# Kernel tuning notes

Measured on AMD Instinct MI355X. Metric: run time of the kernel, lower is better.

The kernel has to match this reference:

```python
import jax, jax.numpy as jnp
import numpy as np

B, N = 4, 8192
D = 128
DEPTH = 4
LEAF = 32
HEADS = 4
HD = D // HEADS
SLOTS = 24
RANKS = [20, 32, 52, 82]                      # rank at encoder step j (fine -> coarse)
EXP = [RANKS[j] * (2 ** j) for j in range(DEPTH)]  # HODLR head output dims


def _rope_tables(seq_len, dim):
    inv_freq = 1.0 / (10000.0 ** (jnp.arange(0, dim, 2, dtype=jnp.float32) / dim))
    t = jnp.arange(seq_len, dtype=jnp.float32)
    freqs = t[:, None] * inv_freq[None, :]
    emb = jnp.concatenate([freqs, freqs], axis=-1)   # [S, dim]
    return jnp.cos(emb), jnp.sin(emb)


def _rotate_half(x):
    x1, x2 = jnp.split(x, 2, axis=-1)
    return jnp.concatenate([-x2, x1], axis=-1)


def _layernorm(x, g, b, eps=1e-5):
    mu = jnp.mean(x, -1, keepdims=True)
    var = jnp.mean((x - mu) ** 2, -1, keepdims=True)
    return (x - mu) * jax.lax.rsqrt(var + eps) * g + b


def _block_attn(h, qkv_w, qkv_b, pw, pb, cos, sin):
    Bc, Nc, C = h.shape
    nb = Nc // LEAF
    xb = h.reshape(Bc * nb, LEAF, C)
    qkv = (xb @ qkv_w + qkv_b).reshape(Bc * nb, LEAF, 3, HEADS, HD)
    qkv = qkv.transpose(2, 0, 3, 1, 4)               # [3, BN, H, L, hd]
    q, k, v = qkv[0], qkv[1], qkv[2]
    q = q * cos + _rotate_half(q) * sin              # full-dim RoPE (rope_dim == head_dim)
    k = k * cos + _rotate_half(k) * sin
    attn = jax.nn.softmax(jnp.einsum('bhqd,bhkd->bhqk', q, k) * (HD ** -0.5), axis=-1)
    o = jnp.einsum('bhqk,bhkd->bhqd', attn, v).transpose(0, 2, 1, 3).reshape(Bc * nb, LEAF, C)
    return (o @ pw + pb).reshape(Bc, Nc, C)


def _forward(x, cen_w, cen_b, nbr_w, nbr_b, inp_w, inp_b,
             leafp_w, leafp_b, leafh_w, leafh_b, log_scale_leaf,
             ln1_g, ln1_b, qkv_w, qkv_b, attnp_w, attnp_b,
             ln2_g, ln2_b, mlp1_w, mlp1_b, mlp2_w, mlp2_b, ds_w, ds_b,
             hu_w0, hu_b0, hv_w0, hv_b0, hu_w1, hu_b1, hv_w1, hv_b1,
             hu_w2, hu_b2, hv_w2, hv_b2, hu_w3, hu_b3, hv_w3, hv_b3):
    Bx, Nx, _ = x.shape
    # --- SymmetricNeighborEmbed (24 neighbor slots, vectorized) ---
    pos_i = x[..., 0:3]
    diag_i = x[..., 3:4]
    h_center = jnp.concatenate([pos_i, diag_i], -1) @ cen_w + cen_b          # [B,N,D]
    nb_feat = x[..., 4:4 + 5 * SLOTS].reshape(Bx, Nx, SLOTS, 5)
    rel = nb_feat[..., 0:1]
    pos_j = nb_feat[..., 1:4]
    w_ij = nb_feat[..., 4:5]
    active = (w_ij != 0.0).astype(x.dtype)
    feat = jnp.concatenate([rel * active, (pos_j - pos_i[:, :, None, :]) * active, w_ij], -1)
    e = (feat @ nbr_w + nbr_b) * active                                       # [B,N,24,D]
    h = h_center + jnp.sum(e, axis=2)
    h = h @ inp_w + inp_b
    # --- leaf dense diagonal blocks ---
    nl = Nx // LEAF
    hl = h.reshape(Bx, nl, LEAF, D) @ leafp_w + leafp_b                       # [B,nl,32,32]
    u_leaf = hl @ leafh_w + leafh_b
    dense = jnp.einsum('blik,bljk->blij', u_leaf, u_leaf) * jnp.exp(log_scale_leaf)
    diag_a = x[..., 3]                                                        # scale_A defaults to 1.0
    mask = jnp.abs(diag_a) > 1e-6
    new_diag = jnp.where(mask, 1.0 / jnp.where(mask, diag_a, 1.0), 1.0).reshape(Bx, nl, LEAF)
    dense = dense + new_diag[..., :, None] * jnp.eye(LEAF, dtype=x.dtype)
    # --- down-only encoder: transformer block -> HODLR head -> 2:1 downsample ---
    cos, sin = _rope_tables(LEAF, HD)
    hu = [(hu_w0, hu_b0), (hu_w1, hu_b1), (hu_w2, hu_b2), (hu_w3, hu_b3)]
    hv = [(hv_w0, hv_b0), (hv_w1, hv_b1), (hv_w2, hv_b2), (hv_w3, hv_b3)]
    us, vs = [], []
    for j in range(DEPTH):
        a = _block_attn(_layernorm(h, ln1_g[j], ln1_b[j]),
                        qkv_w[j], qkv_b[j], attnp_w[j], attnp_b[j], cos, sin)
        h = h + a
        m = _layernorm(h, ln2_g[j], ln2_b[j])
        m = jax.nn.gelu(m @ mlp1_w[j] + mlp1_b[j], approximate=False) @ mlp2_w[j] + mlp2_b[j]
        h = h + m
        us.append((h @ hu[j][0] + hu[j][1]).reshape(Bx, Nx, RANKS[j]))
        vs.append((h @ hv[j][0] + hv[j][1]).reshape(Bx, Nx, RANKS[j]))
        Bh, n, c = h.shape
        h = h.reshape(Bh, n // 2, 2 * c) @ ds_w[j] + ds_b[j]
    # single flat output: dense leaf blocks + all U/V HODLR factors
    return jnp.concatenate([dense.reshape(Bx, -1),
                            jnp.concatenate(us, -1).reshape(Bx, -1),
                            jnp.concatenate(vs, -1).reshape(Bx, -1)], -1)


def setup_inputs():
    key = jax.random.key(0)
    ks = iter(jax.random.split(key, 64))
    def rn(shape, s=0.05):
        return jax.random.normal(next(ks), shape, jnp.float32) * s
    z = lambda *s: jnp.zeros(s, jnp.float32)
    o = lambda *s: jnp.ones(s, jnp.float32)
    inp = {
        'x': jax.random.normal(next(ks), (B, N, 4 + 5 * SLOTS), jnp.float32),
        'cen_w': rn((4, D)), 'cen_b': z(D),
        'nbr_w': rn((5, D)), 'nbr_b': z(D),
        'inp_w': rn((D, D)), 'inp_b': z(D),
        'leafp_w': rn((D, LEAF)), 'leafp_b': z(LEAF),
        'leafh_w': rn((LEAF, LEAF), 0.01), 'leafh_b': z(LEAF),
        'log_scale_leaf': jnp.full((1,), np.log(0.01), jnp.float32),
        'ln1_g': o(DEPTH, D), 'ln1_b': z(DEPTH, D),
        'qkv_w': rn((DEPTH, D, 3 * D)), 'qkv_b': z(DEPTH, 3 * D),
        'attnp_w': rn((DEPTH, D, D)), 'attnp_b': z(DEPTH, D),
        'ln2_g': o(DEPTH, D), 'ln2_b': z(DEPTH, D),
        'mlp1_w': rn((DEPTH, D, 4 * D)), 'mlp1_b': z(DEPTH, 4 * D),
        'mlp2_w': rn((DEPTH, 4 * D, D)), 'mlp2_b': z(DEPTH, D),
        'ds_w': rn((DEPTH, 2 * D, D)), 'ds_b': z(DEPTH, D),
    }
    for j in range(DEPTH):
        inp['hu_w%d' % j] = rn((D, EXP[j]), 0.01)
        inp['hu_b%d' % j] = z(EXP[j])
        inp['hv_w%d' % j] = rn((D, EXP[j]), 0.01)
        inp['hv_b%d' % j] = z(EXP[j])
    return inp


def reference(x, cen_w, cen_b, nbr_w, nbr_b, inp_w, inp_b,
              leafp_w, leafp_b, leafh_w, leafh_b, log_scale_leaf,
              ln1_g, ln1_b, qkv_w, qkv_b, attnp_w, attnp_b,
              ln2_g, ln2_b, mlp1_w, mlp1_b, mlp2_w, mlp2_b, ds_w, ds_b,
              hu_w0, hu_b0, hv_w0, hv_b0, hu_w1, hu_b1, hv_w1, hv_b1,
              hu_w2, hu_b2, hv_w2, hv_b2, hu_w3, hu_b3, hv_w3, hv_b3):
    return _forward(x, cen_w, cen_b, nbr_w, nbr_b, inp_w, inp_b,
                    leafp_w, leafp_b, leafh_w, leafh_b, log_scale_leaf,
                    ln1_g, ln1_b, qkv_w, qkv_b, attnp_w, attnp_b,
                    ln2_g, ln2_b, mlp1_w, mlp1_b, mlp2_w, mlp2_b, ds_w, ds_b,
                    hu_w0, hu_b0, hv_w0, hv_b0, hu_w1, hu_b1, hv_w1, hv_b1,
                    hu_w2, hu_b2, hv_w2, hv_b2, hu_w3, hu_b3, hv_w3, hv_b3)
```

## Files before the change

### kernel.cpp

```cpp
#include <hip/hip_runtime.h>
#include <hip/hip_bf16.h>
#include <math.h>

#define DEV __device__ __forceinline__

constexpr int XFv = 124;
constexpr size_t OPB   = 3309568;
constexpr size_t UBASE = 262144;
constexpr size_t VBASE = 1785856;
constexpr int UVWID = 186;

using bfrag  = __attribute__((ext_vector_type(8))) short;
using f32x4v = __attribute__((ext_vector_type(4))) float;

DEV float* at4p(float* base, int t, int c0, int W) {
  return base + t * W + ((c0 + 4 * t) & (W - 1));
}
DEV float& at1r(float* base, int t, int c, int W) {
  return base[t * W + (((c & ~3) + 4 * t) & (W - 1)) + (c & 3)];
}
DEV float4 ld4g(const float* p) { return *(const float4*)p; }
DEV void fma4(float4& a, float s, const float4& w) {
  a.x += s * w.x; a.y += s * w.y; a.z += s * w.z; a.w += s * w.w;
}
DEV float gelu_fast(float x) {
  float x2 = x * x;
  float z = x * (1.5957691216057308f + 0.0713551f * x2);
  float e = __expf(z);
  float r = 1.0f - __frcp_rn(e + 1.0f);
  return x * r;
}
DEV ushort f2bf(float x) {
  __hip_bfloat16 b = __float2bfloat16(x);
  union { __hip_bfloat16 h; ushort u; } cv;
  cv.h = b;
  return cv.u;
}
DEV unsigned f2bf2(float lo, float hi) {
  __hip_bfloat162 b2 = __float22bfloat162_rn(make_float2(lo, hi));
  union { __hip_bfloat162 h; unsigned u; } cv;
  cv.h = b2;
  return cv.u;
}
DEV void stb128(ushort* b, int row, int col, float v) {
  b[row * 128 + (((col & ~7) + 8 * row) & 127) + (col & 7)] = f2bf(v);
}

__global__ __launch_bounds__(256) void wprep_all_kernel(
    const float* __restrict__ src0, ushort* __restrict__ dst0, int K, int N) {
  size_t off = (size_t)blockIdx.z * K * N;
  const float* src = src0 + off;
  ushort* dst = dst0 + off;
  __shared__ float S[64][65];
  int tid = threadIdx.x;
  int k0 = blockIdx.x * 64, n0 = blockIdx.y * 64;
  for (int i = tid; i < 64 * 64; i += 256) {
    int kk = i >> 6, nn = i & 63;
    S[kk][nn] = src[(size_t)(k0 + kk) * N + n0 + nn];
  }
  __syncthreads();
  int n = tid >> 2, kq = tid & 3;
  unsigned pk[8];
#pragma unroll
  for (int i = 0; i < 8; i++) {
    int k = kq * 16 + 2 * i;
    pk[i] = f2bf2(S[k][n], S[k + 1][n]);
  }
  unsigned* dp = (unsigned*)&dst[(size_t)(n0 + n) * K + k0 + kq * 16];
#pragma unroll
  for (int i = 0; i < 8; i++) dp[i] = pk[i];
}

struct UVDesc {
  const float* src[8];
  ushort* dst[8];
  int expj[8];
  int npad[8];
};
__global__ __launch_bounds__(256) void uvprep_all_kernel(UVDesc d) {
  int mi = blockIdx.y;
  int i = blockIdx.x * 256 + threadIdx.x;
  int expj = d.expj[mi];
  if (i >= d.npad[mi] * 128) return;
  int n = i >> 7, k = i & 127;
  d.dst[mi][(size_t)n * 128 + k] =
      (n < expj) ? f2bf(d.src[mi][(size_t)k * expj + n]) : (ushort)0;
}

__global__ __launch_bounds__(128) void weff_prep_kernel(
    const float* __restrict__ cw, const float* __restrict__ cb,
    const float* __restrict__ nw, const float* __restrict__ nb,
    const float* __restrict__ iw, const float* __restrict__ ib,
    float* __restrict__ weff, float* __restrict__ ropetab) {
  __shared__ float S[11 * 128];
  int tid = threadIdx.x;
  for (int i = tid; i < 512; i += 128) S[i] = cw[i];
  for (int i = tid; i < 640; i += 128) S[512 + i] = nw[i];
  S[1152 + tid] = nb[tid];
  S[1280 + tid] = cb[tid];
  __syncthreads();
  float acc[11];
#pragma unroll
  for (int r = 0; r < 10; r++) acc[r] = 0.f;
  acc[10] = ib[tid];
  for (int k = 0; k < 128; k++) {
    float w = iw[k * 128 + tid];
#pragma unroll
    for (int r = 0; r < 11; r++) acc[r] += S[r * 128 + k] * w;
  }
#pragma unroll
  for (int r = 0; r < 11; r++) weff[r * 128 + tid] = acc[r];
  for (int idx = tid; idx < 512; idx += 128) {
    int pos = idx >> 4, d = idx & 15;
    float ang = (float)pos * expf(-0.57564627324851148f * (float)d);
    ropetab[idx] = cosf(ang);
    ropetab[512 + idx] = sinf(ang);
  }
}

__global__ __launch_bounds__(256) void node_embed2_kernel(
    const float* __restrict__ x, const float* __restrict__ weff,
    float* __restrict__ h) {
  __shared__ float XR[64 * XFv];
  __shared__ float RF[64][11];
  __shared__ __align__(16) float WE[11 * 128];
  int tid = threadIdx.x;
  int node0 = blockIdx.x * 64;
  for (int i = tid; i < 64 * XFv; i += 256)
    XR[i] = x[(size_t)node0 * XFv + i];
  for (int i = tid; i < 11 * 128; i += 256) WE[i] = weff[i];
  __syncthreads();
  {
    int nn = tid >> 2, sl = tid & 3;
    const float* xr = XR + nn * XFv;
    float p0 = xr[0], p1 = xr[1], p2 = xr[2];
    float g[6] = {0.f, 0.f, 0.f, 0.f, 0.f, 0.f};
#pragma unroll
    for (int s = 0; s < 6; s++) {
      const float* f = xr + 4 + 5 * (sl * 6 + s);
      float w = f[4];
      if (w != 0.0f) {
        g[0] += f[0]; g[1] += f[1] - p0; g[2] += f[2] - p1;
        g[3] += f[3] - p2; g[4] += w; g[5] += 1.0f;
      }
    }
#pragma unroll
    for (int i = 0; i < 6; i++) {
      g[i] += __shfl_xor(g[i], 1);
      g[i] += __shfl_xor(g[i], 2);
    }
    if (sl == 0) {
      RF[nn][0] = p0; RF[nn][1] = p1; RF[nn][2] = p2; RF[nn][3] = xr[3];
#pragma unroll
      for (int i = 0; i < 6; i++) RF[nn][4 + i] = g[i];
    }
  }
  __syncthreads();
  {
    int w = tid >> 6, lane = tid & 63;
    int c4 = lane & 31, hi = lane >> 5;
    const float4* WE4 = (const float4*)WE;
#pragma unroll
    for (int rr = 0; rr < 8; rr++) {
      int node = w * 16 + rr * 2 + hi;
      float4 acc = WE4[10 * 32 + c4];
#pragma unroll
      for (int f = 0; f < 10; f++)
        fma4(acc, RF[node][f], WE4[f * 32 + c4]);
      *(float4*)&h[(size_t)(node0 + node) * 128 + c4 * 4] = acc;
    }
  }
}

__global__ __launch_bounds__(256) void leaf_dense_kernel(
    const float* __restrict__ h, const float* __restrict__ x,
    const float* __restrict__ lpw, const float* __restrict__ lpb,
    const float* __restrict__ lhw, const float* __restrict__ lhb,
    const float* __restrict__ lsc, float* __restrict__ out) {
  __shared__ __align__(16) float HS[32 * 128];
  __shared__ __align__(16) float HL[32 * 32];
  __shared__ __align__(16) float UL[32 * 32];
  int tid = threadIdx.x;
  int leaf = blockIdx.x;
  size_t base = (size_t)leaf * (32 * 128);
  for (int i = tid; i < 32 * 128; i += 256) {
    int t = i >> 7, c = i & 127;
    at1r(HS, t, c, 128) = h[base + i];
  }
  __syncthreads();
  int t = tid & 31, cg = tid >> 5;
  {
    float4 acc = ld4g(&lpb[4 * cg]);
    for (int k4 = 0; k4 < 128; k4 += 4) {
      float4 xv = *(const float4*)at4p(HS, t, k4, 128);
      float xa[4] = {xv.x, xv.y, xv.z, xv.w};
#pragma unroll
      for (int kk = 0; kk < 4; kk++)
        fma4(acc, xa[kk], ld4g(&lpw[(k4 + kk) * 32 + 4 * cg]));
    }
    *(float4*)at4p(HL, t, 4 * cg, 32) = acc;
  }
  __syncthreads();
  {
    float4 acc = ld4g(&lhb[4 * cg]);
    for (int k4 = 0; k4 < 32; k4 += 4) {
      float4 xv = *(const float4*)at4p(HL, t, k4, 32);
      float xa[4] = {xv.x, xv.y, xv.z, xv.w};
#pragma unroll
      for (int kk = 0; kk < 4; kk++)
        fma4(acc, xa[kk], ld4g(&lhw[(k4 + kk) * 32 + 4 * cg]));
    }
    *(float4*)at4p(UL, t, 4 * cg, 32) = acc;
  }
  __syncthreads();
  {
    float scale = expf(lsc[0]);
    float acc[4] = {0.f, 0.f, 0.f, 0.f};
    for (int k4 = 0; k4 < 32; k4 += 4) {
      float4 xv = *(const float4*)at4p(UL, t, k4, 32);
      float xa[4] = {xv.x, xv.y, xv.z, xv.w};
#pragma unroll
      for (int kk = 0; kk < 4; kk++) {
        int k = k4 + kk;
#pragma unroll
        for (int i2 = 0; i2 < 4; i2++)
          acc[i2] += xa[kk] * at1r(UL, 4 * cg + i2, k, 32);
      }
    }
    int b = leaf >> 8, l = leaf & 255;
#pragma unroll
    for (int i2 = 0; i2 < 4; i2++) {
      int c = 4 * cg + i2;
      float v = acc[i2] * scale;
      if (c == t) {
        float dg = x[(size_t)(leaf * 32 + t) * XFv + 3];
        v += (fabsf(dg) > 1e-6f) ? (1.0f / dg) : 1.0f;
      }
      out[(size_t)b * OPB + (size_t)l * 1024 + t * 32 + c] = v;
    }
  }
}

__global__ __launch_bounds__(256, 4) void layer_mfma_kernel(
    float* __restrict__ h,
    const float* __restrict__ lng, const float* __restrict__ lnb,
    const ushort* __restrict__ wqkvt, const float* __restrict__ bqkv,
    const ushort* __restrict__ wpt, const float* __restrict__ pb,
    const float* __restrict__ rt,
    const float* __restrict__ ln2g, const float* __restrict__ ln2b,
    const ushort* __restrict__ w1t, const float* __restrict__ b1,
    const ushort* __restrict__ w2t, const float* __restrict__ b2) {
  __shared__ __align__(16) ushort SM[20480];
  ushort* XN = SM;
  ushort* QB = SM + 4096;
  ushort* KB = SM + 8192;
  ushort* VT = SM + 12288;
  ushort* HC1 = SM + 16384;
  float*  HS = (float*)(SM + 8192);
  int tid = threadIdx.x;
  size_t base = (size_t)blockIdx.x * (32 * 128);
  int w = tid >> 6, l = tid & 63, lm = l & 15, q = l >> 4;

  {
    int m8 = tid >> 3, p8 = tid & 7;
    const float* row = h + base + m8 * 128 + p8 * 16;
    float v[16];
    float s = 0.f;
#pragma unroll
    for (int i = 0; i < 16; i += 4) {
      float4 t4 = ld4g(row + i);
      v[i] = t4.x; v[i + 1] = t4.y; v[i + 2] = t4.z; v[i + 3] = t4.w;
      s += t4.x + t4.y + t4.z + t4.w;
    }
    s += __shfl_xor(s, 1); s += __shfl_xor(s, 2); s += __shfl_xor(s, 4);
    float mu = s * (1.0f / 128.0f);
    float s2 = 0.f;
#pragma unroll
    for (int i = 0; i < 16; i++) { float d = v[i] - mu; s2 += d * d; }
    s2 += __shfl_xor(s2, 1); s2 += __shfl_xor(s2, 2); s2 += __shfl_xor(s2, 4);
    float rs = rsqrtf(s2 * (1.0f / 128.0f) + 1e-5f);
    unsigned* XW = (unsigned*)XN;
#pragma unroll
    for (int i = 0; i < 16; i += 2) {
      int c = p8 * 16 + i;
      float x0 = (v[i] - mu) * rs * lng[c] + lnb[c];
      float x1 = (v[i + 1] - mu) * rs * lng[c + 1] + lnb[c + 1];
      int kp = c >> 1;
      XW[m8 * 64 + ((kp + 4 * m8) & 63)] = f2bf2(x0, x1);
    }
  }
  __syncthreads();

  {
    f32x4v acc[2][6];
#pragma unroll
    for (int mt = 0; mt < 2; mt++)
#pragma unroll
      for (int nt = 0; nt < 6; nt++) acc[mt][nt] = (f32x4v){0.f, 0.f, 0.f, 0.f};
    for (int ks = 0; ks < 4; ks++) {
      bfrag a[2];
#pragma unroll
      for (int mt = 0; mt < 2; mt++) {
        int mm = mt * 16 + lm;
        a[mt] = *(const bfrag*)&XN[mm * 128 + ((ks * 32 + q * 8 + 8 * mm) & 127)];
      }
#pragma unroll
      for (int nt = 0; nt < 6; nt++) {
        int n = w * 96 + nt * 16 + lm;
        bfrag b = *(const bfrag*)&wqkvt[(size_t)n * 128 + ks * 32 + q * 8];
#pragma unroll
        for (int mt = 0; mt < 2; mt++)
          acc[mt][nt] = __builtin_amdgcn_mfma_f32_16x16x32_bf16(
              a[mt], b, acc[mt][nt], 0, 0, 0);
      }
    }
    float csA[4] = {}, snA[4] = {}, csB[4] = {}, snB[4] = {};
    if (w < 3) {
#pragma unroll
      for (int r = 0; r < 4; r++) {
        int pa = q * 4 + r;
        csA[r] = rt[pa * 16 + lm];        snA[r] = rt[512 + pa * 16 + lm];
        csB[r] = rt[(pa + 16) * 16 + lm]; snB[r] = rt[512 + (pa + 16) * 16 + lm];
      }
    }
#pragma unroll
    for (int p2 = 0; p2 < 3; p2++) {
      int g = w * 6 + 2 * p2;
      int ne = g * 16 + lm;
      if (g < 16) {
        float be = bqkv[ne], bo = bqkv[ne + 16];
        ushort* dst = (g < 8) ? QB : KB;
        int de = (g < 8) ? ne : ne - 128;
#pragma unroll
        for (int mt = 0; mt < 2; mt++)
#pragma unroll
          for (int r = 0; r < 4; r++) {
            int mm = mt * 16 + q * 4 + r;
            float cs = (mt & 1) ? csB[r] : csA[r];
            float sn = (mt & 1) ? snB[r] : snA[r];
            float e = acc[mt][2 * p2][r] + be;
            float o = acc[mt][2 * p2 + 1][r] + bo;
            stb128(dst, mm, de, e * cs - o * sn);
            stb128(dst, mm, de + 16, o * cs + e * sn);
          }
      } else {
#pragma unroll
        for (int h2 = 0; h2 < 2; h2++) {
          int nt = 2 * p2 + h2;
          int nv = (g + h2) * 16 + lm;
          int dv = nv - 256;
          float bv = bqkv[nv];
#pragma unroll
          for (int mt = 0; mt < 2; mt++) {
            int t0 = mt * 16 + q * 4;
            uint2 pk;
            pk.x = f2bf2(acc[mt][nt][0] + bv, acc[mt][nt][1] + bv);
            pk.y = f2bf2(acc[mt][nt][2] + bv, acc[mt][nt][3] + bv);
            *(uint2*)&VT[dv * 32 + (((t0 & ~7) + 8 * dv) & 31) + (t0 & 7)] = pk;
          }
        }
      }
    }
  }
  __syncthreads();

  ushort* SP = XN;
  ushort* OB = QB;
  {
    int head = w;
    {
      f32x4v sc[2][2];
#pragma unroll
      for (int a2 = 0; a2 < 2; a2++)
#pragma unroll
        for (int b2 = 0; b2 < 2; b2++) sc[a2][b2] = (f32x4v){0.f, 0.f, 0.f, 0.f};
      bfrag qa[2], kb[2];
#pragma unroll
      for (int mt2 = 0; mt2 < 2; mt2++) {
        int row = mt2 * 16 + lm;
        qa[mt2] = *(const bfrag*)&QB[row * 128 + ((head * 32 + q * 8 + 8 * row) & 127)];
      }
#pragma unroll
      for (int nt2 = 0; nt2 < 2; nt2++) {
        int kt = nt2 * 16 + lm;
        kb[nt2] = *(const bfrag*)&KB[kt * 128 + ((head * 32 + q * 8 + 8 * kt) & 127)];
      }
#pragma unroll
      for (int mt2 = 0; mt2 < 2; mt2++)
#pragma unroll
        for (int nt2 = 0; nt2 < 2; nt2++)
          sc[mt2][nt2] = __builtin_amdgcn_mfma_f32_16x16x32_bf16(
              qa[mt2], kb[nt2], sc[mt2][nt2], 0, 0, 0);
      const float scl = 0.17677669529663688f;
#pragma unroll
      for (int mt2 = 0; mt2 < 2; mt2++)
#pragma unroll
        for (int nt2 = 0; nt2 < 2; nt2++)
#pragma unroll
          for (int r = 0; r < 4; r++) {
            int qt = mt2 * 16 + q * 4 + r;
            int kc = nt2 * 16 + lm;
            SP[head * 1024 + qt * 32 + (((kc & ~7) + 8 * qt) & 31) + (kc & 7)] =
                f2bf(sc[mt2][nt2][r] * scl);
          }
    }
    {
      int rowid = l >> 1, half = l & 1;
      ushort* rowp = SP + head * 1024 + rowid * 32 + half * 16;
      float v[16];
#pragma unroll
      for (int pc = 0; pc < 2; pc++) {
        uint4 ch = *(const uint4*)&rowp[pc * 8];
        unsigned uu[4] = {ch.x, ch.y, ch.z, ch.w};
#pragma unroll
        for (int i2 = 0; i2 < 4; i2++) {
          v[pc * 8 + 2 * i2]     = __uint_as_float(uu[i2] << 16);
          v[pc * 8 + 2 * i2 + 1] = __uint_as_float(uu[i2] & 0xffff0000u);
        }
      }
      float mx = -1e30f;
#pragma unroll
      for (int i = 0; i < 16; i++) mx = fmaxf(mx, v[i]);
      mx = fmaxf(mx, __shfl_xor(mx, 1));
      float s = 0.f;
#pragma unroll
      for (int i = 0; i < 16; i++) { v[i] = __expf(v[i] - mx); s += v[i]; }
      s += __shfl_xor(s, 1);
      float inv = 1.0f / s;
#pragma unroll
      for (int pc = 0; pc < 2; pc++) {
        uint4 ch;
        unsigned uu[4];
#pragma unroll
        for (int i2 = 0; i2 < 4; i2++)
          uu[i2] = f2bf2(v[pc * 8 + 2 * i2] * inv, v[pc * 8 + 2 * i2 + 1] * inv);
        ch.x = uu[0]; ch.y = uu[1]; ch.z = uu[2]; ch.w = uu[3];
        *(uint4*)&rowp[pc * 8] = ch;
      }
    }
    {
      f32x4v ov[2][2];
#pragma unroll
      for (int a2 = 0; a2 < 2; a2++)
#pragma unroll
        for (int b2 = 0; b2 < 2; b2++) ov[a2][b2] = (f32x4v){0.f, 0.f, 0.f, 0.f};
      bfrag pa[2], vb2[2];
#pragma unroll
      for (int mt2 = 0; mt2 < 2; mt2++) {
        int qt = mt2 * 16 + lm;
        pa[mt2] = *(const bfrag*)&SP[head * 1024 + qt * 32 + ((q * 8 + 8 * qt) & 31)];
      }
#pragma unroll
      for (int nt2 = 0; nt2 < 2; nt2++) {
        int gdim = head * 32 + nt2 * 16 + lm;
        vb2[nt2] = *(const bfrag*)&VT[gdim * 32 + ((q * 8 + 8 * gdim) & 31)];
      }
#pragma unroll
      for (int mt2 = 0; mt2 < 2; mt2++)
#pragma unroll
        for (int nt2 = 0; nt2 < 2; nt2++)
          ov[mt2][nt2] = __builtin_amdgcn_mfma_f32_16x16x32_bf16(
              pa[mt2], vb2[nt2], ov[mt2][nt2], 0, 0, 0);
#pragma unroll
      for (int mt2 = 0; mt2 < 2; mt2++)
#pragma unroll
        for (int nt2 = 0; nt2 < 2; nt2++)
#pragma unroll
          for (int r = 0; r < 4; r++) {
            int qt = mt2 * 16 + q * 4 + r;
            int gdim = head * 32 + nt2 * 16 + lm;
            stb128(OB, qt, gdim, ov[mt2][nt2][r]);
          }
    }
  }
  __syncthreads();

  {
    f32x4v po[2][2];
#pragma unroll
    for (int mt = 0; mt < 2; mt++)
#pragma unroll
      for (int nt = 0; nt < 2; nt++) po[mt][nt] = (f32x4v){0.f, 0.f, 0.f, 0.f};
    for (int ks = 0; ks < 4; ks++) {
      bfrag a[2];
#pragma unroll
      for (int mt = 0; mt < 2; mt++) {
        int mm = mt * 16 + lm;
        a[mt] = *(const bfrag*)&OB[mm * 128 + ((ks * 32 + q * 8 + 8 * mm) & 127)];
      }
#pragma unroll
      for (int nt = 0; nt < 2; nt++) {
        int n = w * 32 + nt * 16 + lm;
        bfrag b = *(const bfrag*)&wpt[(size_t)n * 128 + ks * 32 + q * 8];
#pragma unroll
        for (int mt = 0; mt < 2; mt++)
          po[mt][nt] = __builtin_amdgcn_mfma_f32_16x16x32_bf16(
              a[mt], b, po[mt][nt], 0, 0, 0);
      }
    }
#pragma unroll
    for (int nt = 0; nt < 2; nt++) {
      int n = w * 32 + nt * 16 + lm;
      float bv = pb[n];
#pragma unroll
      for (int mt = 0; mt < 2; mt++)
#pragma unroll
        for (int r = 0; r < 4; r++) {
          int mm = mt * 16 + q * 4 + r;
          at1r(HS, mm, n, 128) = po[mt][nt][r] + bv;
        }
    }
  }
  __syncthreads();

  {
    int j = tid & 31;
    int c0 = j * 4;
    float g0 = ln2g[c0], g1 = ln2g[c0 + 1], g2 = ln2g[c0 + 2], g3 = ln2g[c0 + 3];
    float e0 = ln2b[c0], e1 = ln2b[c0 + 1], e2 = ln2b[c0 + 2], e3 = ln2b[c0 + 3];
    unsigned* XW = (unsigned*)XN;
#pragma unroll
    for (int k2 = 0; k2 < 4; k2++) {
      int idx = tid + 256 * k2;
      int tok = idx >> 5;
      float4 hg = ld4g(&h[base + (size_t)idx * 4]);
      float4 ao = *(const float4*)at4p(HS, tok, 4 * j, 128);
      float4 hn;
      hn.x = hg.x + ao.x; hn.y = hg.y + ao.y;
      hn.z = hg.z + ao.z; hn.w = hg.w + ao.w;
      *(float4*)at4p(HS, tok, 4 * j, 128) = hn;
      float s = hn.x + hn.y + hn.z + hn.w;
      s += __shfl_xor(s, 1); s += __shfl_xor(s, 2); s += __shfl_xor(s, 4);
      s += __shfl_xor(s, 8); s += __shfl_xor(s, 16);
      float mu = s * (1.0f / 128.0f);
      float d0 = hn.x - mu, d1 = hn.y - mu, d2 = hn.z - mu, d3 = hn.w - mu;
      float s2 = d0 * d0 + d1 * d1 + d2 * d2 + d3 * d3;
      s2 += __shfl_xor(s2, 1); s2 += __shfl_xor(s2, 2); s2 += __shfl_xor(s2, 4);
      s2 += __shfl_xor(s2, 8); s2 += __shfl_xor(s2, 16);
      float rs = rsqrtf(s2 * (1.0f / 128.0f) + 1e-5f);
      float x0 = d0 * rs * g0 + e0;
      float x1 = d1 * rs * g1 + e1;
      float x2 = d2 * rs * g2 + e2;
      float x3 = d3 * rs * g3 + e3;
      int kp = 2 * j;
      XW[tok * 64 + ((kp + 4 * tok) & 63)] = f2bf2(x0, x1);
      XW[tok * 64 + ((kp + 1 + 4 * tok) & 63)] = f2bf2(x2, x3);
    }
  }
  __syncthreads();

  ushort* HC0 = QB;
  f32x4v acc2[2][2];
#pragma unroll
  for (int mt = 0; mt < 2; mt++)
#pragma unroll
    for (int nt = 0; nt < 2; nt++) acc2[mt][nt] = (f32x4v){0.f, 0.f, 0.f, 0.f};

  auto mlp1_calc = [&](int hc, f32x4v A1[2][2]) {
#pragma unroll
    for (int mt = 0; mt < 2; mt++)
#pragma unroll
      for (int nt = 0; nt < 2; nt++) A1[mt][nt] = (f32x4v){0.f, 0.f, 0.f, 0.f};
#pragma unroll
    for (int ks = 0; ks < 4; ks++) {
      bfrag a[2];
#pragma unroll
      for (int mt = 0; mt < 2; mt++) {
        int mm = mt * 16 + lm;
        a[mt] = *(const bfrag*)&XN[mm * 128 + ((ks * 32 + q * 8 + 8 * mm) & 127)];
      }
#pragma unroll
      for (int nt = 0; nt < 2; nt++) {
        int n = hc * 128 + w * 32 + nt * 16 + lm;
        bfrag b = *(const bfrag*)&w1t[(size_t)n * 128 + ks * 32 + q * 8];
#pragma unroll
        for (int mt = 0; mt < 2; mt++)
          A1[mt][nt] = __builtin_amdgcn_mfma_f32_16x16x32_bf16(
              a[mt], b, A1[mt][nt], 0, 0, 0);
      }
    }
  };
  auto gelu_store = [&](int hc, f32x4v A1[2][2], ushort* HCd) {
#pragma unroll
    for (int nt = 0; nt < 2; nt++) {
      int nl = w * 32 + nt * 16 + lm;
      float b1v = b1[hc * 128 + nl];
#pragma unroll
      for (int mt = 0; mt < 2; mt++)
#pragma unroll
        for (int r = 0; r < 4; r++) {
          int mm = mt * 16 + q * 4 + r;
          float val = gelu_fast(A1[mt][nt][r] + b1v);
          HCd[mm * 128 + (((nl & ~7) + 8 * mm) & 127) + (nl & 7)] = f2bf(val);
        }
    }
  };
  auto mlp2_calc = [&](int hc, ushort* HCr) {
#pragma unroll
    for (int ks = 0; ks < 4; ks++) {
      bfrag a[2];
#pragma unroll
      for (int mt = 0; mt < 2; mt++) {
        int mm = mt * 16 + lm;
        a[mt] = *(const bfrag*)&HCr[mm * 128 + ((ks * 32 + q * 8 + 8 * mm) & 127)];
      }
#pragma unroll
      for (int nt = 0; nt < 2; nt++) {
        int n = w * 32 + nt * 16 + lm;
        bfrag b = *(const bfrag*)&w2t[(size_t)n * 512 + hc * 128 + ks * 32 + q * 8];
#pragma unroll
        for (int mt = 0; mt < 2; mt++)
          acc2[mt][nt] = __builtin_amdgcn_mfma_f32_16x16x32_bf16(
              a[mt], b, acc2[mt][nt], 0, 0, 0);
      }
    }
  };

  f32x4v a1A[2][2], a1B[2][2];
  mlp1_calc(0, a1A);
  gelu_store(0, a1A, HC0);
  __syncthreads();
  mlp1_calc(1, a1B);
  mlp2_calc(0, HC0);
  gelu_store(1, a1B, HC1);
  __syncthreads();
  mlp1_calc(2, a1A);
  mlp2_calc(1, HC1);
  gelu_store(2, a1A, HC0);
  __syncthreads();
  mlp1_calc(3, a1B);
  mlp2_calc(2, HC0);
  gelu_store(3, a1B, HC1);
  __syncthreads();
  mlp2_calc(3, HC1);

#pragma unroll
  for (int nt = 0; nt < 2; nt++) {
    int n = w * 32 + nt * 16 + lm;
    float b2v = b2[n];
#pragma unroll
    for (int mt = 0; mt < 2; mt++)
#pragma unroll
      for (int r = 0; r < 4; r++) {
        int mm = mt * 16 + q * 4 + r;
        h[base + (size_t)mm * 128 + n] = at1r(HS, mm, n, 128) + acc2[mt][nt][r] + b2v;
      }
  }
}

template <int EXPJ, int RANK, int LVL, int NSPLIT>
__global__ __launch_bounds__(256) void uvds_kernel(
    const float* __restrict__ h,
    const ushort* __restrict__ uwt, const float* __restrict__ ub,
    const ushort* __restrict__ vwt, const float* __restrict__ vb,
    float* __restrict__ ustg, float* __restrict__ vstg,
    float* __restrict__ hout,
    const ushort* __restrict__ dwt, const float* __restrict__ dsb) {
  constexpr int NT16 = (EXPJ + 15) / 16;
  constexpr int NJOBS = 2 * NT16;
  __shared__ __align__(16) ushort XN[64 * 128];
  int tid = threadIdx.x;
  int t0 = blockIdx.x * 64;
  size_t base = (size_t)t0 * 128;
  {
    int m = tid >> 2, p = tid & 3;
    const float* row = h + base + m * 128 + p * 32;
    unsigned* XW = (unsigned*)XN;
#pragma unroll
    for (int i = 0; i < 32; i += 4) {
      float4 t4 = ld4g(row + i);
      int kp = (p * 32 + i) >> 1;
      XW[m * 64 + ((kp + 4 * m) & 63)] = f2bf2(t4.x, t4.y);
      XW[m * 64 + ((kp + 1 + 4 * m) & 63)] = f2bf2(t4.z, t4.w);
    }
  }
  __syncthreads();
  int w = tid >> 6, l = tid & 63, lm = l & 15, q = l >> 4;
  int gw = w + 4 * blockIdx.y;
  for (int jj = gw; jj < NJOBS; jj += 4 * NSPLIT) {
    int uvsel = jj & 1, nt = jj >> 1;
    const ushort* wt = uvsel ? vwt : uwt;
    const float* bias = uvsel ? vb : ub;
    float* stg = uvsel ? vstg : ustg;
    f32x4v acc[4];
#pragma unroll
    for (int mt = 0; mt < 4; mt++) acc[mt] = (f32x4v){0.f, 0.f, 0.f, 0.f};
    for (int ks = 0; ks < 4; ks++) {
      bfrag b = *(const bfrag*)&wt[(size_t)(nt * 16 + lm) * 128 + ks * 32 + q * 8];
#pragma unroll
      for (int mt = 0; mt < 4; mt++) {
        int mm = mt * 16 + lm;
        int ke = ks * 32 + q * 8;
        bfrag a = *(const bfrag*)&XN[mm * 128 + ((ke + 8 * mm) & 127)];
        acc[mt] = __builtin_amdgcn_mfma_f32_16x16x32_bf16(a, b, acc[mt], 0, 0, 0);
      }
    }
    int c = nt * 16 + lm;
    if (c < EXPJ) {
      float bv = bias[c];
#pragma unroll
      for (int mt = 0; mt < 4; mt++)
#pragma unroll
        for (int r = 0; r < 4; r++) {
          int mm = mt * 16 + q * 4 + r;
          stg[(size_t)(t0 + mm) * EXPJ + c] = acc[mt][r] + bv;
        }
    }
  }
  if constexpr (LVL < 3) {
    if (blockIdx.y == 0) {
      f32x4v dacc[2][2];
#pragma unroll
      for (int mt = 0; mt < 2; mt++)
#pragma unroll
        for (int nt = 0; nt < 2; nt++) dacc[mt][nt] = (f32x4v){0.f, 0.f, 0.f, 0.f};
      for (int ks = 0; ks < 8; ks++) {
        bfrag a[2];
#pragma unroll
        for (int mt = 0; mt < 2; mt++) {
          int rr = mt * 16 + lm;
          int tok = 2 * rr + (ks >> 2);
          int c2 = (ks & 3) * 32 + q * 8;
          a[mt] = *(const bfrag*)&XN[tok * 128 + ((c2 + 8 * tok) & 127)];
        }
#pragma unroll
        for (int nt = 0; nt < 2; nt++) {
          int n = w * 32 + nt * 16 + lm;
          bfrag b = *(const bfrag*)&dwt[(size_t)n * 256 + ks * 32 + q * 8];
#pragma unroll
          for (int mt = 0; mt < 2; mt++)
            dacc[mt][nt] = __builtin_amdgcn_mfma_f32_16x16x32_bf16(
                a[mt], b, dacc[mt][nt], 0, 0, 0);
        }
      }
      size_t ob2 = (size_t)blockIdx.x * (32 * 128);
#pragma unroll
      for (int nt = 0; nt < 2; nt++) {
        int n = w * 32 + nt * 16 + lm;
        float bv = dsb[n];
#pragma unroll
        for (int mt = 0; mt < 2; mt++)
#pragma unroll
          for (int r = 0; r < 4; r++) {
            int mm = mt * 16 + q * 4 + r;
            hout[ob2 + (size_t)mm * 128 + n] = dacc[mt][nt][r] + bv;
          }
      }
    }
  }
}

struct StgPtrs { const float* u[4]; const float* v[4]; };
__global__ __launch_bounds__(256) void uv_assemble_kernel(
    StgPtrs sp, float* __restrict__ out) {
  __shared__ unsigned char JL[93];
  __shared__ unsigned char CM[93];
  int tid = threadIdx.x;
  if (tid < 93) {
    int c = 2 * tid;
    int j = (c < 20) ? 0 : (c < 52) ? 1 : (c < 104) ? 2 : 3;
    int coff = (j == 0) ? 0 : (j == 1) ? 20 : (j == 2) ? 52 : 104;
    JL[tid] = (unsigned char)j;
    CM[tid] = (unsigned char)(c - coff);
  }
  __syncthreads();
  int g0 = blockIdx.x * 32;
  for (int i = tid; i < 32 * 93; i += 256) {
    int rr = i / 93, cp = i - rr * 93;
    int g = g0 + rr;
    int b = g >> 13, n = g & 8191;
    int j = JL[cp], cm = CM[cp];
    int expj, rank;
    if (j == 0)      { expj = 20;  rank = 20; }
    else if (j == 1) { expj = 64;  rank = 32; }
    else if (j == 2) { expj = 208; rank = 52; }
    else             { expj = 656; rank = 82; }
    int tok = (b << (13 - j)) + (n >> j);
    int cdiv = n & ((1 << j) - 1);
    size_t si = (size_t)tok * expj + cdiv * rank + cm;
    size_t ob = (size_t)b * OPB + (size_t)n * UVWID + 2 * cp;
    *(float2*)&out[ob + UBASE] = *(const float2*)&sp.u[j][si];
    *(float2*)&out[ob + VBASE] = *(const float2*)&sp.v[j][si];
  }
}

extern "C" void kernel_launch(void* const* d_in, const int* in_sizes, int n_in,
                              void* d_out, int out_size, void* d_ws, size_t ws_size,
                              hipStream_t stream) {
  const float* x       = (const float*)d_in[0];
  const float* cen_w   = (const float*)d_in[1];
  const float* cen_b   = (const float*)d_in[2];
  const float* nbr_w   = (const float*)d_in[3];
  const float* nbr_b   = (const float*)d_in[4];
  const float* inp_w   = (const float*)d_in[5];
  const float* inp_b   = (const float*)d_in[6];
  const float* leafp_w = (const float*)d_in[7];
  const float* leafp_b = (const float*)d_in[8];
  const float* leafh_w = (const float*)d_in[9];
  const float* leafh_b = (const float*)d_in[10];
  const float* lscale  = (const float*)d_in[11];
  const float* ln1_g   = (const float*)d_in[12];
  const float* ln1_b   = (const float*)d_in[13];
  const float* qkv_w   = (const float*)d_in[14];
  const float* qkv_b   = (const float*)d_in[15];
  const float* attnp_w = (const float*)d_in[16];
  const float* attnp_b = (const float*)d_in[17];
  const float* ln2_g   = (const float*)d_in[18];
  const float* ln2_b   = (const float*)d_in[19];
  const float* mlp1_w  = (const float*)d_in[20];
  const float* mlp1_b  = (const float*)d_in[21];
  const float* mlp2_w  = (const float*)d_in[22];
  const float* mlp2_b  = (const float*)d_in[23];
  const float* ds_w    = (const float*)d_in[24];
  const float* ds_b    = (const float*)d_in[25];
  const float* huw[4], *hub[4], *hvw[4], *hvb[4];
  for (int j = 0; j < 4; j++) {
    huw[j] = (const float*)d_in[26 + 4 * j];
    hub[j] = (const float*)d_in[27 + 4 * j];
    hvw[j] = (const float*)d_in[28 + 4 * j];
    hvb[j] = (const float*)d_in[29 + 4 * j];
  }
  float* out = (float*)d_out;
  float* hA = (float*)d_ws;
  float* hB = hA + (size_t)4 * 8192 * 128;
  ushort* w1t = (ushort*)(hB + (size_t)2097152);
  ushort* w2t = w1t + (size_t)4 * 65536;
  ushort* uvt = w2t + (size_t)4 * 65536;
  const int NPAD[4] = {32, 64, 208, 656};
  ushort* uwt[4]; ushort* vwt[4];
  ushort* p = uvt;
  for (int j = 0; j < 4; j++) {
    uwt[j] = p; p += (size_t)NPAD[j] * 128;
    vwt[j] = p; p += (size_t)NPAD[j] * 128;
  }
  ushort* wqkvt = p;
  ushort* wpt   = wqkvt + (size_t)4 * 384 * 128;
  ushort* dswt  = wpt + (size_t)4 * 128 * 128;
  float* weff   = (float*)(dswt + (size_t)4 * 128 * 256);
  float* ropetab = weff + 1408;
  const size_t STG[4] = {32768ull * 20, 16384ull * 64, 8192ull * 208, 4096ull * 656};
  float* ustg[4]; float* vstg[4];
  float* sp2 = ropetab + 1024;
  for (int j = 0; j < 4; j++) {
    ustg[j] = sp2; sp2 += STG[j];
    vstg[j] = sp2; sp2 += STG[j];
  }
  const int EXPJ_[4] = {20, 64, 208, 656};

  weff_prep_kernel<<<1, 128, 0, stream>>>(
      cen_w, cen_b, nbr_w, nbr_b, inp_w, inp_b, weff, ropetab);
  wprep_all_kernel<<<dim3(2, 8, 4), 256, 0, stream>>>(mlp1_w, w1t, 128, 512);
  wprep_all_kernel<<<dim3(8, 2, 4), 256, 0, stream>>>(mlp2_w, w2t, 512, 128);
  wprep_all_kernel<<<dim3(2, 6, 4), 256, 0, stream>>>(qkv_w, wqkvt, 128, 384);
  wprep_all_kernel<<<dim3(2, 2, 4), 256, 0, stream>>>(attnp_w, wpt, 128, 128);
  wprep_all_kernel<<<dim3(4, 2, 4), 256, 0, stream>>>(ds_w, dswt, 256, 128);
  {
    UVDesc d;
    for (int j = 0; j < 4; j++) {
      d.src[2 * j] = huw[j];     d.dst[2 * j] = uwt[j];
      d.src[2 * j + 1] = hvw[j]; d.dst[2 * j + 1] = vwt[j];
      d.expj[2 * j] = EXPJ_[j];  d.expj[2 * j + 1] = EXPJ_[j];
      d.npad[2 * j] = NPAD[j];   d.npad[2 * j + 1] = NPAD[j];
    }
    uvprep_all_kernel<<<dim3(328, 8), 256, 0, stream>>>(d);
  }

  node_embed2_kernel<<<(4 * 8192) / 64, 256, 0, stream>>>(x, weff, hA);
  leaf_dense_kernel<<<(4 * 8192) / 32, 256, 0, stream>>>(
      hA, x, leafp_w, leafp_b, leafh_w, leafh_b, lscale, out);

  layer_mfma_kernel<<<32768 / 32, 256, 0, stream>>>(
      hA, ln1_g, ln1_b, wqkvt, qkv_b, wpt, attnp_b, ropetab,
      ln2_g, ln2_b, w1t, mlp1_b, w2t, mlp2_b);
  uvds_kernel<20, 20, 0, 1><<<dim3(512, 1), 256, 0, stream>>>(
      hA, uwt[0], hub[0], vwt[0], hvb[0], ustg[0], vstg[0],
      hB, dswt, ds_b);

  layer_mfma_kernel<<<16384 / 32, 256, 0, stream>>>(
      hB, ln1_g + 128, ln1_b + 128, wqkvt + 49152, qkv_b + 384,
      wpt + 16384, attnp_b + 128, ropetab,
      ln2_g + 128, ln2_b + 128, w1t + 65536, mlp1_b + 512,
      w2t + 65536, mlp2_b + 128);
  uvds_kernel<64, 32, 1, 2><<<dim3(256, 2), 256, 0, stream>>>(
      hB, uwt[1], hub[1], vwt[1], hvb[1], ustg[1], vstg[1],
      hA, dswt + 32768, ds_b + 128);

  layer_mfma_kernel<<<8192 / 32, 256, 0, stream>>>(
      hA, ln1_g + 256, ln1_b + 256, wqkvt + 98304, qkv_b + 768,
      wpt + 32768, attnp_b + 256, ropetab,
      ln2_g + 256, ln2_b + 256, w1t + 131072, mlp1_b + 1024,
      w2t + 131072, mlp2_b + 256);
  uvds_kernel<208, 52, 2, 4><<<dim3(128, 4), 256, 0, stream>>>(
      hA, uwt[2], hub[2], vwt[2], hvb[2], ustg[2], vstg[2],
      hB, dswt + 65536, ds_b + 256);

  layer_mfma_kernel<<<4096 / 32, 256, 0, stream>>>(
      hB, ln1_g + 384, ln1_b + 384, wqkvt + 147456, qkv_b + 1152,
      wpt + 49152, attnp_b + 384, ropetab,
      ln2_g + 384, ln2_b + 384, w1t + 196608, mlp1_b + 1536,
      w2t + 196608, mlp2_b + 384);
  uvds_kernel<656, 82, 3, 8><<<dim3(64, 8), 256, 0, stream>>>(
      hB, uwt[3], hub[3], vwt[3], hvb[3], ustg[3], vstg[3],
      hA , dswt , ds_b );

  {
    StgPtrs sp;
    for (int j = 0; j < 4; j++) { sp.u[j] = ustg[j]; sp.v[j] = vstg[j]; }
    uv_assemble_kernel<<<32768 / 32, 256, 0, stream>>>(sp, out);
  }
  (void)in_sizes; (void)n_in; (void)out_size; (void)ws_size;
}
```

Before: 426.3 us.

## Split downsample from UV heads and co-schedule UV heads with next encoder layer

The downsample projection is split out of the UV-head kernel into its own small kernel. The UV-head projection for level j now runs in the same grid as the transformer layer for level j+1, with blocks branching on blockIdx, so the two independent workloads can fill the GPU together on the smaller coarse-level grids. The UV-head kernel also gets a launch bound of 4. This saves launches and idle tail time but adds a separate ds launch, makes the combined kernel use the larger shared-memory footprint for UV blocks, and relies on the two branches sharing one register budget.

```diff
diff --git a/kernel.cpp b/kernel.cpp
--- a/kernel.cpp
+++ b/kernel.cpp
@@ -241,7 +241,7 @@
   }
 }
 
-__global__ __launch_bounds__(256, 4) void layer_mfma_kernel(
+DEV void layer_body(ushort* SM, int tid, int bid,
     float* __restrict__ h,
     const float* __restrict__ lng, const float* __restrict__ lnb,
     const ushort* __restrict__ wqkvt, const float* __restrict__ bqkv,
@@ -250,15 +250,13 @@
     const float* __restrict__ ln2g, const float* __restrict__ ln2b,
     const ushort* __restrict__ w1t, const float* __restrict__ b1,
     const ushort* __restrict__ w2t, const float* __restrict__ b2) {
-  __shared__ __align__(16) ushort SM[20480];
   ushort* XN = SM;
   ushort* QB = SM + 4096;
   ushort* KB = SM + 8192;
   ushort* VT = SM + 12288;
   ushort* HC1 = SM + 16384;
   float*  HS = (float*)(SM + 8192);
-  int tid = threadIdx.x;
-  size_t base = (size_t)blockIdx.x * (32 * 128);
+  size_t base = (size_t)bid * (32 * 128);
   int w = tid >> 6, l = tid & 63, lm = l & 15, q = l >> 4;
 
   {
@@ -648,19 +646,16 @@
   }
 }
 
-template <int EXPJ, int RANK, int LVL, int NSPLIT>
-__global__ __launch_bounds__(256) void uvds_kernel(
+template <int EXPJ, int RANK, int NSPLIT>
+DEV void uv_body(ushort* XN, int tid, int ubid, int nx,
     const float* __restrict__ h,
     const ushort* __restrict__ uwt, const float* __restrict__ ub,
     const ushort* __restrict__ vwt, const float* __restrict__ vb,
-    float* __restrict__ ustg, float* __restrict__ vstg,
-    float* __restrict__ hout,
-    const ushort* __restrict__ dwt, const float* __restrict__ dsb) {
+    float* __restrict__ ustg, float* __restrict__ vstg) {
   constexpr int NT16 = (EXPJ + 15) / 16;
   constexpr int NJOBS = 2 * NT16;
-  __shared__ __align__(16) ushort XN[64 * 128];
-  int tid = threadIdx.x;
-  int t0 = blockIdx.x * 64;
+  int bx = ubid % nx, by = ubid / nx;
+  int t0 = bx * 64;
   size_t base = (size_t)t0 * 128;
   {
     int m = tid >> 2, p = tid & 3;
@@ -676,7 +671,7 @@
   }
   __syncthreads();
   int w = tid >> 6, l = tid & 63, lm = l & 15, q = l >> 4;
-  int gw = w + 4 * blockIdx.y;
+  int gw = w + 4 * by;
   for (int jj = gw; jj < NJOBS; jj += 4 * NSPLIT) {
     int uvsel = jj & 1, nt = jj >> 1;
     const ushort* wt = uvsel ? vwt : uwt;
@@ -707,46 +702,116 @@
         }
     }
   }
-  if constexpr (LVL < 3) {
-    if (blockIdx.y == 0) {
-      f32x4v dacc[2][2];
+}
+
+__global__ __launch_bounds__(256, 4) void layer_mfma_kernel(
+    float* __restrict__ h,
+    const float* __restrict__ lng, const float* __restrict__ lnb,
+    const ushort* __restrict__ wqkvt, const float* __restrict__ bqkv,
+    const ushort* __restrict__ wpt, const float* __restrict__ pb,
+    const float* __restrict__ rt,
+    const float* __restrict__ ln2g, const float* __restrict__ ln2b,
+    const ushort* __restrict__ w1t, const float* __restrict__ b1,
+    const ushort* __restrict__ w2t, const float* __restrict__ b2) {
+  __shared__ __align__(16) ushort SM[20480];
+  layer_body(SM, threadIdx.x, blockIdx.x, h, lng, lnb, wqkvt, bqkv, wpt, pb,
+             rt, ln2g, ln2b, w1t, b1, w2t, b2);
+}
+
+template <int EXPJ, int RANK, int NSPLIT>
+__global__ __launch_bounds__(256, 4) void combo_kernel(
+    float* __restrict__ h,
+    const float* __restrict__ lng, const float* __restrict__ lnb,
+    const ushort* __restrict__ wqkvt, const float* __restrict__ bqkv,
+    const ushort* __restrict__ wpt, const float* __restrict__ pb,
+    const float* __restrict__ rt,
+    const float* __restrict__ ln2g, const float* __restrict__ ln2b,
+    const ushort* __restrict__ w1t, const float* __restrict__ b1,
+    const ushort* __restrict__ w2t, const float* __restrict__ b2,
+    int nLayer,
+    const float* __restrict__ hprev,
+    const ushort* __restrict__ uwt, const float* __restrict__ ub,
+    const ushort* __restrict__ vwt, const float* __restrict__ vb,
+    float* __restrict__ ustg, float* __restrict__ vstg, int nx) {
+  __shared__ __align__(16) ushort SM[20480];
+  int tid = threadIdx.x;
+  if ((int)blockIdx.x < nLayer) {
+    layer_body(SM, tid, blockIdx.x, h, lng, lnb, wqkvt, bqkv, wpt, pb,
+               rt, ln2g, ln2b, w1t, b1, w2t, b2);
+  } else {
+    uv_body<EXPJ, RANK, NSPLIT>(SM, tid, (int)blockIdx.x - nLayer, nx,
+                                hprev, uwt, ub, vwt, vb, ustg, vstg);
+  }
+}
+
+template <int EXPJ, int RANK, int NSPLIT>
+__global__ __launch_bounds__(256, 4) void uv_kernel(
+    const float* __restrict__ h,
+    const ushort* __restrict__ uwt, const float* __restrict__ ub,
+    const ushort* __restrict__ vwt, const float* __restrict__ vb,
+    float* __restrict__ ustg, float* __restrict__ vstg, int nx) {
+  __shared__ __align__(16) ushort XN[64 * 128];
+  uv_body<EXPJ, RANK, NSPLIT>(XN, threadIdx.x, blockIdx.x, nx,
+                              h, uwt, ub, vwt, vb, ustg, vstg);
+}
+
+__global__ __launch_bounds__(256) void ds_kernel(
+    const float* __restrict__ h, float* __restrict__ hout,
+    const ushort* __restrict__ dwt, const float* __restrict__ dsb) {
+  __shared__ __align__(16) ushort XN[64 * 128];
+  int tid = threadIdx.x;
+  int t0 = blockIdx.x * 64;
+  size_t base = (size_t)t0 * 128;
+  {
+    int m = tid >> 2, p = tid & 3;
+    const float* row = h + base + m * 128 + p * 32;
+    unsigned* XW = (unsigned*)XN;
+#pragma unroll
+    for (int i = 0; i < 32; i += 4) {
+      float4 t4 = ld4g(row + i);
+      int kp = (p * 32 + i) >> 1;
+      XW[m * 64 + ((kp + 4 * m) & 63)] = f2bf2(t4.x, t4.y);
+      XW[m * 64 + ((kp + 1 + 4 * m) & 63)] = f2bf2(t4.z, t4.w);
+    }
+  }
+  __syncthreads();
+  int w = tid >> 6, l = tid & 63, lm = l & 15, q = l >> 4;
+  f32x4v dacc[2][2];
+#pragma unroll
+  for (int mt = 0; mt < 2; mt++)
+#pragma unroll
+    for (int nt = 0; nt < 2; nt++) dacc[mt][nt] = (f32x4v){0.f, 0.f, 0.f, 0.f};
+  for (int ks = 0; ks < 8; ks++) {
+    bfrag a[2];
+#pragma unroll
+    for (int mt = 0; mt < 2; mt++) {
+      int rr = mt * 16 + lm;
+      int tok = 2 * rr + (ks >> 2);
+      int c2 = (ks & 3) * 32 + q * 8;
+      a[mt] = *(const bfrag*)&XN[tok * 128 + ((c2 + 8 * tok) & 127)];
+    }
+#pragma unroll
+    for (int nt = 0; nt < 2; nt++) {
+      int n = w * 32 + nt * 16 + lm;
+      bfrag b = *(const bfrag*)&dwt[(size_t)n * 256 + ks * 32 + q * 8];
 #pragma unroll
       for (int mt = 0; mt < 2; mt++)
-#pragma unroll
-        for (int nt = 0; nt < 2; nt++) dacc[mt][nt] = (f32x4v){0.f, 0.f, 0.f, 0.f};
-      for (int ks = 0; ks < 8; ks++) {
-        bfrag a[2];
-#pragma unroll
-        for (int mt = 0; mt < 2; mt++) {
-          int rr = mt * 16 + lm;
-          int tok = 2 * rr + (ks >> 2);
-          int c2 = (ks & 3) * 32 + q * 8;
-          a[mt] = *(const bfrag*)&XN[tok * 128 + ((c2 + 8 * tok) & 127)];
-        }
-#pragma unroll
-        for (int nt = 0; nt < 2; nt++) {
-          int n = w * 32 + nt * 16 + lm;
-          bfrag b = *(const bfrag*)&dwt[(size_t)n * 256 + ks * 32 + q * 8];
-#pragma unroll
-          for (int mt = 0; mt < 2; mt++)
-            dacc[mt][nt] = __builtin_amdgcn_mfma_f32_16x16x32_bf16(
-                a[mt], b, dacc[mt][nt], 0, 0, 0);
-        }
-      }
-      size_t ob2 = (size_t)blockIdx.x * (32 * 128);
-#pragma unroll
-      for (int nt = 0; nt < 2; nt++) {
-        int n = w * 32 + nt * 16 + lm;
-        float bv = dsb[n];
-#pragma unroll
-        for (int mt = 0; mt < 2; mt++)
-#pragma unroll
-          for (int r = 0; r < 4; r++) {
-            int mm = mt * 16 + q * 4 + r;
-            hout[ob2 + (size_t)mm * 128 + n] = dacc[mt][nt][r] + bv;
-          }
-      }
-    }
+        dacc[mt][nt] = __builtin_amdgcn_mfma_f32_16x16x32_bf16(
+            a[mt], b, dacc[mt][nt], 0, 0, 0);
+    }
+  }
+  size_t ob2 = (size_t)blockIdx.x * (32 * 128);
+#pragma unroll
+  for (int nt = 0; nt < 2; nt++) {
+    int n = w * 32 + nt * 16 + lm;
+    float bv = dsb[n];
+#pragma unroll
+    for (int mt = 0; mt < 2; mt++)
+#pragma unroll
+      for (int r = 0; r < 4; r++) {
+        int mm = mt * 16 + q * 4 + r;
+        hout[ob2 + (size_t)mm * 128 + n] = dacc[mt][nt][r] + bv;
+      }
   }
 }
 
@@ -872,36 +937,33 @@
   layer_mfma_kernel<<<32768 / 32, 256, 0, stream>>>(
       hA, ln1_g, ln1_b, wqkvt, qkv_b, wpt, attnp_b, ropetab,
       ln2_g, ln2_b, w1t, mlp1_b, w2t, mlp2_b);
-  uvds_kernel<20, 20, 0, 1><<<dim3(512, 1), 256, 0, stream>>>(
-      hA, uwt[0], hub[0], vwt[0], hvb[0], ustg[0], vstg[0],
-      hB, dswt, ds_b);
-
-  layer_mfma_kernel<<<16384 / 32, 256, 0, stream>>>(
+  ds_kernel<<<512, 256, 0, stream>>>(hA, hB, dswt, ds_b);
+
+  combo_kernel<20, 20, 1><<<512 + 512, 256, 0, stream>>>(
       hB, ln1_g + 128, ln1_b + 128, wqkvt + 49152, qkv_b + 384,
       wpt + 16384, attnp_b + 128, ropetab,
       ln2_g + 128, ln2_b + 128, w1t + 65536, mlp1_b + 512,
-      w2t + 65536, mlp2_b + 128);
-  uvds_kernel<64, 32, 1, 2><<<dim3(256, 2), 256, 0, stream>>>(
-      hB, uwt[1], hub[1], vwt[1], hvb[1], ustg[1], vstg[1],
-      hA, dswt + 32768, ds_b + 128);
-
-  layer_mfma_kernel<<<8192 / 32, 256, 0, stream>>>(
+      w2t + 65536, mlp2_b + 128, 512,
+      hA, uwt[0], hub[0], vwt[0], hvb[0], ustg[0], vstg[0], 512);
+  ds_kernel<<<256, 256, 0, stream>>>(hB, hA, dswt + 32768, ds_b + 128);
+
+  combo_kernel<64, 32, 2><<<256 + 512, 256, 0, stream>>>(
       hA, ln1_g + 256, ln1_b + 256, wqkvt + 98304, qkv_b + 768,
       wpt + 32768, attnp_b + 256, ropetab,
       ln2_g + 256, ln2_b + 256, w1t + 131072, mlp1_b + 1024,
-      w2t + 131072, mlp2_b + 256);
-  uvds_kernel<208, 52, 2, 4><<<dim3(128, 4), 256, 0, stream>>>(
-      hA, uwt[2], hub[2], vwt[2], hvb[2], ustg[2], vstg[2],
-      hB, dswt + 65536, ds_b + 256);
-
-  layer_mfma_kernel<<<4096 / 32, 256, 0, stream>>>(
+      w2t + 131072, mlp2_b + 256, 256,
+      hB, uwt[1], hub[1], vwt[1], hvb[1], ustg[1], vstg[1], 256);
+  ds_kernel<<<128, 256, 0, stream>>>(hA, hB, dswt + 65536, ds_b + 256);
+
+  combo_kernel<208, 52, 4><<<128 + 512, 256, 0, stream>>>(
       hB, ln1_g + 384, ln1_b + 384, wqkvt + 147456, qkv_b + 1152,
       wpt + 49152, attnp_b + 384, ropetab,
       ln2_g + 384, ln2_b + 384, w1t + 196608, mlp1_b + 1536,
-      w2t + 196608, mlp2_b + 384);
-  uvds_kernel<656, 82, 3, 8><<<dim3(64, 8), 256, 0, stream>>>(
-      hB, uwt[3], hub[3], vwt[3], hvb[3], ustg[3], vstg[3],
-      hA , dswt , ds_b );
+      w2t + 196608, mlp2_b + 384, 128,
+      hA, uwt[2], hub[2], vwt[2], hvb[2], ustg[2], vstg[2], 128);
+
+  uv_kernel<656, 82, 8><<<512, 256, 0, stream>>>(
+      hB, uwt[3], hub[3], vwt[3], hvb[3], ustg[3], vstg[3], 64);
 
   {
     StgPtrs sp;
```

Measured after the change: 588.5 us. 1.38x slower.
